# Kernel optimization log

Measured on AMD Instinct MI355X. Metric: run time of the kernel, lower is better.

## Reference

```python
import jax, jax.numpy as jnp
import numpy as np

B, S, H, E = 32, 4096, 512, 512
NEG = -1000000000.0


def setup_inputs() -> dict:
    key = jax.random.key(0)
    ks = jax.random.split(key, 8)
    query = jax.random.normal(ks[0], (B, H), dtype=jnp.float32)
    keys = jax.random.normal(ks[1], (B, S, E), dtype=jnp.float32)
    mask = jax.random.randint(ks[2], (B, S), 0, 2, dtype=jnp.int32)
    # learned params (torch Linear: y = x @ W.T + b); store W already transposed
    Wq = jax.random.normal(ks[3], (H, H), dtype=jnp.float32) / np.sqrt(H)
    bq = jnp.zeros((H,), dtype=jnp.float32)
    Wk = jax.random.normal(ks[4], (E, H), dtype=jnp.float32) / np.sqrt(E)
    bk = jnp.zeros((H,), dtype=jnp.float32)
    v = jax.random.normal(ks[5], (H,), dtype=jnp.float32) / np.sqrt(H)
    bv = jnp.zeros((), dtype=jnp.float32)
    return {"query": query, "keys": keys, "mask": mask,
            "Wq": Wq, "bq": bq, "Wk": Wk, "bk": bk, "v": v, "bv": bv}


def reference(query, keys, mask, Wq, bq, Wk, bk, v, bv):
    # q_proj: (B, 1, H); k_proj: (B, S, H)
    q_proj = (query @ Wq + bq)[:, None, :]
    k_proj = jnp.einsum('bse,eh->bsh', keys, Wk) + bk
    # additive score: v^T tanh(q + k) + bv -> (B, S)
    scores = jnp.einsum('bsh,h->bs', jnp.tanh(q_proj + k_proj), v) + bv
    scores = jnp.where(mask == 0, NEG, scores)
    attn = jax.nn.softmax(scores, axis=-1)          # (B, S)
    context = jnp.einsum('bs,bse->be', attn, keys)  # (B, E)
    return context, attn
```

## Files before the change

### kernel.cpp

```cpp
#include <hip/hip_runtime.h>
#include <hip/hip_bf16.h>

#define BB 32
#define SS 4096
#define HH 512
#define EE 512
#define NEGV -1000000000.0f

using float4v = __attribute__((ext_vector_type(4))) float;
using short8v = __attribute__((ext_vector_type(8))) short;
using short4v = __attribute__((ext_vector_type(4))) short;

__device__ inline unsigned short f2bf(float x) {
    union { float f; unsigned int u; } c; c.f = x;
    unsigned int r = c.u + 0x7FFFu + ((c.u >> 16) & 1u);
    return (unsigned short)(r >> 16);
}

__global__ void qproj_kernel(const float* __restrict__ query, const float* __restrict__ Wq,
                             float* __restrict__ qp) {
    __shared__ float qs[128];
    int b = blockIdx.y, e0 = blockIdx.x * 128, t = threadIdx.x;
    if (t < 128) qs[t] = query[b * HH + e0 + t];
    __syncthreads();
    int h0 = t, h1 = t + 256;
    float a0 = 0.f, a1 = 0.f;
    for (int e = 0; e < 128; ++e) {
        float q = qs[e];
        a0 += q * Wq[(size_t)(e0 + e) * HH + h0];
        a1 += q * Wq[(size_t)(e0 + e) * HH + h1];
    }
    atomicAdd(&qp[b * HH + h0], a0);
    atomicAdd(&qp[b * HH + h1], a1);
}

__global__ void wkt_kernel(const float* __restrict__ Wk, unsigned short* __restrict__ WkT) {
    int g = blockIdx.x * 256 + threadIdx.x;
    int lane = g & 63, nt = (g >> 6) & 31, ks = g >> 11;
    int lq = lane >> 4, lr = lane & 15;
    int h = nt * 16 + lr;
    int e0 = ks * 32 + lq * 8;
    short8v o;
    #pragma unroll
    for (int j = 0; j < 8; ++j) o[j] = (short)f2bf(Wk[(size_t)(e0 + j) * HH + h]);
    *(short8v*)(WkT + (size_t)g * 8) = o;
}

__launch_bounds__(512, 4)
__global__ void scores_kernel(const float* __restrict__ keys, const unsigned short* __restrict__ WkT,
                              const float* __restrict__ qp, const float* __restrict__ bq,
                              const float* __restrict__ bk, const float* __restrict__ v,
                              const float* __restrict__ bv, const int* __restrict__ mask,
                              float* __restrict__ scores) {
    constexpr int LDK = 264;
    __shared__ unsigned short klds[64 * LDK];
    __shared__ float qp_lds[HH];
    __shared__ float v_lds[HH];
    __shared__ float red[8][64];
    int b = blockIdx.y, s0 = blockIdx.x * 64;
    int tid = threadIdx.x;

    for (int i = tid; i < HH; i += 512) {
        qp_lds[i] = qp[b * HH + i] + bq[i] + bk[i];
        v_lds[i] = v[i];
    }

    int w = tid >> 6, lane = tid & 63;
    int lq = lane >> 4, lr = lane & 15;
    int nt0 = w * 4;

    float4v acc[4][4];
    #pragma unroll
    for (int m = 0; m < 4; ++m)
        #pragma unroll
        for (int j = 0; j < 4; ++j) acc[m][j] = (float4v){0.f, 0.f, 0.f, 0.f};

    const short8v* Wf = (const short8v*)WkT;

    for (int kc = 0; kc < 2; ++kc) {
        __syncthreads();
        const float4v* ksrc = (const float4v*)(keys + ((size_t)b * SS + s0) * EE + kc * 256);
        for (int i = tid; i < 64 * 64; i += 512) {
            int row = i >> 6, c4 = i & 63;
            float4v kv = ksrc[(size_t)row * 128 + c4];
            short4v p;
            p.x = (short)f2bf(kv.x); p.y = (short)f2bf(kv.y);
            p.z = (short)f2bf(kv.z); p.w = (short)f2bf(kv.w);
            *(short4v*)(&klds[row * LDK + c4 * 4]) = p;
        }
        __syncthreads();

        #pragma unroll
        for (int ks = 0; ks < 8; ++ks) {
            int ksg = kc * 8 + ks;
            short8v bfrag[4];
            #pragma unroll
            for (int j = 0; j < 4; ++j)
                bfrag[j] = Wf[((size_t)ksg * 32 + nt0 + j) * 64 + lane];
            #pragma unroll
            for (int m = 0; m < 4; ++m) {
                short8v afrag = *(const short8v*)(&klds[(m * 16 + lr) * LDK + ks * 32 + lq * 8]);
                #pragma unroll
                for (int j = 0; j < 4; ++j)
                    acc[m][j] = __builtin_amdgcn_mfma_f32_16x16x32_bf16(afrag, bfrag[j], acc[m][j], 0, 0, 0);
            }
        }
    }

    float part[4][4];
    #pragma unroll
    for (int m = 0; m < 4; ++m)
        #pragma unroll
        for (int r = 0; r < 4; ++r) part[m][r] = 0.f;
    #pragma unroll
    for (int j = 0; j < 4; ++j) {
        int h = (nt0 + j) * 16 + lr;
        float vj = v_lds[h], qj = qp_lds[h];
        #pragma unroll
        for (int m = 0; m < 4; ++m) {
            #pragma unroll
            for (int r = 0; r < 4; ++r) {
                float x = qj + acc[m][j][r];
                x = fminf(fmaxf(x, -12.f), 12.f);
                float e2 = __expf(2.f * x);
                part[m][r] += vj * ((e2 - 1.f) / (e2 + 1.f));
            }
        }
    }

    #pragma unroll
    for (int m = 0; m < 4; ++m)
        #pragma unroll
        for (int r = 0; r < 4; ++r) {
            float p = part[m][r];
            p += __shfl_xor(p, 1, 16);
            p += __shfl_xor(p, 2, 16);
            p += __shfl_xor(p, 4, 16);
            p += __shfl_xor(p, 8, 16);
            part[m][r] = p;
        }
    if (lr == 0) {
        #pragma unroll
        for (int m = 0; m < 4; ++m)
            #pragma unroll
            for (int r = 0; r < 4; ++r)
                red[w][m * 16 + lq * 4 + r] = part[m][r];
    }
    __syncthreads();
    if (tid < 64) {
        float sc = red[0][tid] + red[1][tid] + red[2][tid] + red[3][tid]
                 + red[4][tid] + red[5][tid] + red[6][tid] + red[7][tid] + bv[0];
        int s = s0 + tid;
        if (mask[b * SS + s] == 0) sc = NEGV;
        scores[b * SS + s] = sc;
    }
}

__global__ void softmax_kernel(const float* __restrict__ scores, float* __restrict__ attn) {
    __shared__ float red[1024];
    int b = blockIdx.x, t = threadIdx.x;
    float s_[4], e_[4];
    float lmax = -3e38f;
    #pragma unroll
    for (int i = 0; i < 4; ++i) { s_[i] = scores[b * SS + t + i * 1024]; lmax = fmaxf(lmax, s_[i]); }
    red[t] = lmax; __syncthreads();
    for (int off = 512; off > 0; off >>= 1) {
        if (t < off) red[t] = fmaxf(red[t], red[t + off]);
        __syncthreads();
    }
    float mx = red[0]; __syncthreads();
    float lsum = 0.f;
    #pragma unroll
    for (int i = 0; i < 4; ++i) { e_[i] = __expf(s_[i] - mx); lsum += e_[i]; }
    red[t] = lsum; __syncthreads();
    for (int off = 512; off > 0; off >>= 1) {
        if (t < off) red[t] += red[t + off];
        __syncthreads();
    }
    float inv = 1.f / red[0];
    #pragma unroll
    for (int i = 0; i < 4; ++i) attn[b * SS + t + i * 1024] = e_[i] * inv;
}

__launch_bounds__(256)
__global__ void context_kernel(const float* __restrict__ keys, const float* __restrict__ attn,
                               float* __restrict__ ctx) {
    __shared__ float a_s[128];
    int chunk = blockIdx.x, b = blockIdx.y, t = threadIdx.x;
    if (t < 128) a_s[t] = attn[b * SS + chunk * 128 + t];
    __syncthreads();
    const float* kbase = keys + ((size_t)b * SS + (size_t)chunk * 128) * EE;
    int e0 = (t & 127) * 4, sr = t >> 7;
    float4v a0 = (float4v){0.f,0.f,0.f,0.f}, a1 = a0, a2 = a0, a3 = a0;
    for (int ss = sr; ss < 128; ss += 8) {
        float4v k0 = *(const float4v*)(kbase + (size_t)(ss    ) * EE + e0);
        float4v k1 = *(const float4v*)(kbase + (size_t)(ss + 2) * EE + e0);
        float4v k2 = *(const float4v*)(kbase + (size_t)(ss + 4) * EE + e0);
        float4v k3 = *(const float4v*)(kbase + (size_t)(ss + 6) * EE + e0);
        float c0 = a_s[ss], c1 = a_s[ss + 2], c2 = a_s[ss + 4], c3 = a_s[ss + 6];
        a0.x += c0*k0.x; a0.y += c0*k0.y; a0.z += c0*k0.z; a0.w += c0*k0.w;
        a1.x += c1*k1.x; a1.y += c1*k1.y; a1.z += c1*k1.z; a1.w += c1*k1.w;
        a2.x += c2*k2.x; a2.y += c2*k2.y; a2.z += c2*k2.z; a2.w += c2*k2.w;
        a3.x += c3*k3.x; a3.y += c3*k3.y; a3.z += c3*k3.z; a3.w += c3*k3.w;
    }
    float4v s4;
    s4.x = (a0.x + a1.x) + (a2.x + a3.x);
    s4.y = (a0.y + a1.y) + (a2.y + a3.y);
    s4.z = (a0.z + a1.z) + (a2.z + a3.z);
    s4.w = (a0.w + a1.w) + (a2.w + a3.w);
    atomicAdd(&ctx[b * EE + e0 + 0], s4.x);
    atomicAdd(&ctx[b * EE + e0 + 1], s4.y);
    atomicAdd(&ctx[b * EE + e0 + 2], s4.z);
    atomicAdd(&ctx[b * EE + e0 + 3], s4.w);
}

extern "C" void kernel_launch(void* const* d_in, const int* in_sizes, int n_in,
                              void* d_out, int out_size, void* d_ws, size_t ws_size,
                              hipStream_t stream) {
    const float* query = (const float*)d_in[0];
    const float* keys  = (const float*)d_in[1];
    const int*   mask  = (const int*)d_in[2];
    const float* Wq    = (const float*)d_in[3];
    const float* bq    = (const float*)d_in[4];
    const float* Wk    = (const float*)d_in[5];
    const float* bk    = (const float*)d_in[6];
    const float* v     = (const float*)d_in[7];
    const float* bv    = (const float*)d_in[8];

    float* out  = (float*)d_out;
    float* ctx  = out;
    float* attn = out + BB * EE;

    char* ws = (char*)d_ws;
    float* qp = (float*)ws;
    unsigned short* WkT = (unsigned short*)(ws + 65536);
    float* scores = (float*)(ws + 65536 + 524288);

    hipMemsetAsync(ctx, 0, BB * EE * sizeof(float), stream);
    hipMemsetAsync(qp, 0, BB * HH * sizeof(float), stream);
    qproj_kernel<<<dim3(4, BB), 256, 0, stream>>>(query, Wq, qp);
    wkt_kernel<<<128, 256, 0, stream>>>(Wk, WkT);
    scores_kernel<<<dim3(SS / 64, BB), 512, 0, stream>>>(keys, WkT, qp, bq, bk, v, bv, mask, scores);
    softmax_kernel<<<BB, 1024, 0, stream>>>(scores, attn);
    context_kernel<<<dim3(SS / 128, BB), 256, 0, stream>>>(keys, attn, ctx);
}
```

Baseline: 509.2 us.

## Double-buffer keys tiles in scores kernel and deepen context/qproj unrolling

The scores kernel now splits the K dimension into four 128-wide chunks held in two LDS buffers. The next chunk's global loads are issued into registers before the current chunk's MFMAs and written to LDS afterwards, so global latency overlaps compute. Separately, the context kernel keeps 8 independent accumulators and loads for more memory-level parallelism, and qproj is split across twice as many blocks with an unrolled loop. This adds register pressure, which could reduce occupancy under the launch bounds.

```diff
diff --git a/kernel.cpp b/kernel.cpp
--- a/kernel.cpp
+++ b/kernel.cpp
@@ -19,13 +19,14 @@
 
 __global__ void qproj_kernel(const float* __restrict__ query, const float* __restrict__ Wq,
                              float* __restrict__ qp) {
-    __shared__ float qs[128];
-    int b = blockIdx.y, e0 = blockIdx.x * 128, t = threadIdx.x;
-    if (t < 128) qs[t] = query[b * HH + e0 + t];
+    __shared__ float qs[64];
+    int b = blockIdx.y, e0 = blockIdx.x * 64, t = threadIdx.x;
+    if (t < 64) qs[t] = query[b * HH + e0 + t];
     __syncthreads();
     int h0 = t, h1 = t + 256;
     float a0 = 0.f, a1 = 0.f;
-    for (int e = 0; e < 128; ++e) {
+    #pragma unroll 8
+    for (int e = 0; e < 64; ++e) {
         float q = qs[e];
         a0 += q * Wq[(size_t)(e0 + e) * HH + h0];
         a1 += q * Wq[(size_t)(e0 + e) * HH + h1];
@@ -52,8 +53,9 @@
                               const float* __restrict__ bk, const float* __restrict__ v,
                               const float* __restrict__ bv, const int* __restrict__ mask,
                               float* __restrict__ scores) {
-    constexpr int LDK = 264;
-    __shared__ unsigned short klds[64 * LDK];
+    constexpr int LDK = 136;
+    constexpr int BUF = 64 * LDK;
+    __shared__ unsigned short klds[2 * BUF];
     __shared__ float qp_lds[HH];
     __shared__ float v_lds[HH];
     __shared__ float red[8][64];
@@ -65,6 +67,22 @@
         v_lds[i] = v[i];
     }
 
+    const float4v* ksrc = (const float4v*)(keys + ((size_t)b * SS + s0) * EE);
+    int r0 = tid >> 5, c4 = tid & 31;
+
+    float4v kreg[4];
+    #pragma unroll
+    for (int p = 0; p < 4; ++p)
+        kreg[p] = ksrc[(size_t)(p * 16 + r0) * 128 + c4];
+    #pragma unroll
+    for (int p = 0; p < 4; ++p) {
+        short4v pk;
+        pk.x = (short)f2bf(kreg[p].x); pk.y = (short)f2bf(kreg[p].y);
+        pk.z = (short)f2bf(kreg[p].z); pk.w = (short)f2bf(kreg[p].w);
+        *(short4v*)(&klds[(p * 16 + r0) * LDK + c4 * 4]) = pk;
+    }
+    __syncthreads();
+
     int w = tid >> 6, lane = tid & 63;
     int lq = lane >> 4, lr = lane & 15;
     int nt0 = w * 4;
@@ -77,34 +95,39 @@
 
     const short8v* Wf = (const short8v*)WkT;
 
-    for (int kc = 0; kc < 2; ++kc) {
-        __syncthreads();
-        const float4v* ksrc = (const float4v*)(keys + ((size_t)b * SS + s0) * EE + kc * 256);
-        for (int i = tid; i < 64 * 64; i += 512) {
-            int row = i >> 6, c4 = i & 63;
-            float4v kv = ksrc[(size_t)row * 128 + c4];
-            short4v p;
-            p.x = (short)f2bf(kv.x); p.y = (short)f2bf(kv.y);
-            p.z = (short)f2bf(kv.z); p.w = (short)f2bf(kv.w);
-            *(short4v*)(&klds[row * LDK + c4 * 4]) = p;
-        }
-        __syncthreads();
-
-        #pragma unroll
-        for (int ks = 0; ks < 8; ++ks) {
-            int ksg = kc * 8 + ks;
+    for (int c = 0; c < 4; ++c) {
+        unsigned cur = (c & 1) * BUF;
+        if (c < 3) {
+            #pragma unroll
+            for (int p = 0; p < 4; ++p)
+                kreg[p] = ksrc[(size_t)(p * 16 + r0) * 128 + (c + 1) * 32 + c4];
+        }
+        #pragma unroll
+        for (int ks = 0; ks < 4; ++ks) {
+            int ksg = c * 4 + ks;
             short8v bfrag[4];
             #pragma unroll
             for (int j = 0; j < 4; ++j)
                 bfrag[j] = Wf[((size_t)ksg * 32 + nt0 + j) * 64 + lane];
             #pragma unroll
             for (int m = 0; m < 4; ++m) {
-                short8v afrag = *(const short8v*)(&klds[(m * 16 + lr) * LDK + ks * 32 + lq * 8]);
+                short8v afrag = *(const short8v*)(&klds[cur + (m * 16 + lr) * LDK + ks * 32 + lq * 8]);
                 #pragma unroll
                 for (int j = 0; j < 4; ++j)
                     acc[m][j] = __builtin_amdgcn_mfma_f32_16x16x32_bf16(afrag, bfrag[j], acc[m][j], 0, 0, 0);
             }
         }
+        if (c < 3) {
+            unsigned nxt = ((c + 1) & 1) * BUF;
+            #pragma unroll
+            for (int p = 0; p < 4; ++p) {
+                short4v pk;
+                pk.x = (short)f2bf(kreg[p].x); pk.y = (short)f2bf(kreg[p].y);
+                pk.z = (short)f2bf(kreg[p].z); pk.w = (short)f2bf(kreg[p].w);
+                *(short4v*)(&klds[nxt + (p * 16 + r0) * LDK + c4 * 4]) = pk;
+            }
+        }
+        __syncthreads();
     }
 
     float part[4][4];
@@ -191,23 +214,26 @@
     __syncthreads();
     const float* kbase = keys + ((size_t)b * SS + (size_t)chunk * 128) * EE;
     int e0 = (t & 127) * 4, sr = t >> 7;
-    float4v a0 = (float4v){0.f,0.f,0.f,0.f}, a1 = a0, a2 = a0, a3 = a0;
-    for (int ss = sr; ss < 128; ss += 8) {
-        float4v k0 = *(const float4v*)(kbase + (size_t)(ss    ) * EE + e0);
-        float4v k1 = *(const float4v*)(kbase + (size_t)(ss + 2) * EE + e0);
-        float4v k2 = *(const float4v*)(kbase + (size_t)(ss + 4) * EE + e0);
-        float4v k3 = *(const float4v*)(kbase + (size_t)(ss + 6) * EE + e0);
-        float c0 = a_s[ss], c1 = a_s[ss + 2], c2 = a_s[ss + 4], c3 = a_s[ss + 6];
-        a0.x += c0*k0.x; a0.y += c0*k0.y; a0.z += c0*k0.z; a0.w += c0*k0.w;
-        a1.x += c1*k1.x; a1.y += c1*k1.y; a1.z += c1*k1.z; a1.w += c1*k1.w;
-        a2.x += c2*k2.x; a2.y += c2*k2.y; a2.z += c2*k2.z; a2.w += c2*k2.w;
-        a3.x += c3*k3.x; a3.y += c3*k3.y; a3.z += c3*k3.z; a3.w += c3*k3.w;
+    float4v a[8];
+    #pragma unroll
+    for (int u = 0; u < 8; ++u) a[u] = (float4v){0.f, 0.f, 0.f, 0.f};
+    for (int ss = sr; ss < 128; ss += 16) {
+        float4v k[8];
+        #pragma unroll
+        for (int u = 0; u < 8; ++u)
+            k[u] = *(const float4v*)(kbase + (size_t)(ss + 2 * u) * EE + e0);
+        #pragma unroll
+        for (int u = 0; u < 8; ++u) {
+            float cw = a_s[ss + 2 * u];
+            a[u].x += cw * k[u].x; a[u].y += cw * k[u].y;
+            a[u].z += cw * k[u].z; a[u].w += cw * k[u].w;
+        }
     }
     float4v s4;
-    s4.x = (a0.x + a1.x) + (a2.x + a3.x);
-    s4.y = (a0.y + a1.y) + (a2.y + a3.y);
-    s4.z = (a0.z + a1.z) + (a2.z + a3.z);
-    s4.w = (a0.w + a1.w) + (a2.w + a3.w);
+    s4.x = ((a[0].x + a[1].x) + (a[2].x + a[3].x)) + ((a[4].x + a[5].x) + (a[6].x + a[7].x));
+    s4.y = ((a[0].y + a[1].y) + (a[2].y + a[3].y)) + ((a[4].y + a[5].y) + (a[6].y + a[7].y));
+    s4.z = ((a[0].z + a[1].z) + (a[2].z + a[3].z)) + ((a[4].z + a[5].z) + (a[6].z + a[7].z));
+    s4.w = ((a[0].w + a[1].w) + (a[2].w + a[3].w)) + ((a[4].w + a[5].w) + (a[6].w + a[7].w));
     atomicAdd(&ctx[b * EE + e0 + 0], s4.x);
     atomicAdd(&ctx[b * EE + e0 + 1], s4.y);
     atomicAdd(&ctx[b * EE + e0 + 2], s4.z);
@@ -238,7 +264,7 @@
 
     hipMemsetAsync(ctx, 0, BB * EE * sizeof(float), stream);
     hipMemsetAsync(qp, 0, BB * HH * sizeof(float), stream);
-    qproj_kernel<<<dim3(4, BB), 256, 0, stream>>>(query, Wq, qp);
+    qproj_kernel<<<dim3(8, BB), 256, 0, stream>>>(query, Wq, qp);
     wkt_kernel<<<128, 256, 0, stream>>>(Wk, WkT);
     scores_kernel<<<dim3(SS / 64, BB), 512, 0, stream>>>(keys, WkT, qp, bq, bk, v, bv, mask, scores);
     softmax_kernel<<<BB, 1024, 0, stream>>>(scores, attn);
```

New measurement: 487.7 us. 4.2% less time.

## Fuse scores, softmax and context into one pass with flash-style partial softmax

Applied to the files above, without the earlier changes.

The scores kernel now stages the full 64x512 key tile in LDS as bf16. It computes local softmax stats (max and sum) per 64-row chunk and accumulates an unnormalized partial context from the same LDS tile, so keys are read from HBM only once. A small finalize kernel rescales the chunk partials, writes ctx and attn, and replaces the separate softmax and context kernels and their atomics. This adds a bf16 rounding of keys in the context product, larger LDS use that lowers occupancy, and a tweak to the qproj split.

```diff
diff --git a/kernel.cpp b/kernel.cpp
--- a/kernel.cpp
+++ b/kernel.cpp
@@ -5,6 +5,7 @@
 #define SS 4096
 #define HH 512
 #define EE 512
+#define NCH 64
 #define NEGV -1000000000.0f
 
 using float4v = __attribute__((ext_vector_type(4))) float;
@@ -16,16 +17,21 @@
     unsigned int r = c.u + 0x7FFFu + ((c.u >> 16) & 1u);
     return (unsigned short)(r >> 16);
 }
+__device__ inline float bf2f(unsigned short s) {
+    union { float f; unsigned int u; } c; c.u = ((unsigned int)s) << 16;
+    return c.f;
+}
 
 __global__ void qproj_kernel(const float* __restrict__ query, const float* __restrict__ Wq,
                              float* __restrict__ qp) {
-    __shared__ float qs[128];
-    int b = blockIdx.y, e0 = blockIdx.x * 128, t = threadIdx.x;
-    if (t < 128) qs[t] = query[b * HH + e0 + t];
+    __shared__ float qs[64];
+    int b = blockIdx.y, e0 = blockIdx.x * 64, t = threadIdx.x;
+    if (t < 64) qs[t] = query[b * HH + e0 + t];
     __syncthreads();
     int h0 = t, h1 = t + 256;
     float a0 = 0.f, a1 = 0.f;
-    for (int e = 0; e < 128; ++e) {
+    #pragma unroll 8
+    for (int e = 0; e < 64; ++e) {
         float q = qs[e];
         a0 += q * Wq[(size_t)(e0 + e) * HH + h0];
         a1 += q * Wq[(size_t)(e0 + e) * HH + h1];
@@ -47,17 +53,19 @@
 }
 
 __launch_bounds__(512, 4)
-__global__ void scores_kernel(const float* __restrict__ keys, const unsigned short* __restrict__ WkT,
-                              const float* __restrict__ qp, const float* __restrict__ bq,
-                              const float* __restrict__ bk, const float* __restrict__ v,
-                              const float* __restrict__ bv, const int* __restrict__ mask,
-                              float* __restrict__ scores) {
-    constexpr int LDK = 264;
+__global__ void fused_kernel(const float* __restrict__ keys, const unsigned short* __restrict__ WkT,
+                             const float* __restrict__ qp, const float* __restrict__ bq,
+                             const float* __restrict__ bk, const float* __restrict__ v,
+                             const float* __restrict__ bv, const int* __restrict__ mask,
+                             float* __restrict__ scores, float* __restrict__ part,
+                             float* __restrict__ marr, float* __restrict__ larr) {
+    constexpr int LDK = EE + 8;
     __shared__ unsigned short klds[64 * LDK];
     __shared__ float qp_lds[HH];
     __shared__ float v_lds[HH];
     __shared__ float red[8][64];
-    int b = blockIdx.y, s0 = blockIdx.x * 64;
+    __shared__ float p_lds[64];
+    int b = blockIdx.y, c = blockIdx.x, s0 = c * 64;
     int tid = threadIdx.x;
 
     for (int i = tid; i < HH; i += 512) {
@@ -65,6 +73,24 @@
         v_lds[i] = v[i];
     }
 
+    const float4v* ksrc = (const float4v*)(keys + ((size_t)b * SS + s0) * EE);
+    #pragma unroll
+    for (int i0 = 0; i0 < 16; i0 += 4) {
+        float4v kv[4];
+        #pragma unroll
+        for (int p = 0; p < 4; ++p) kv[p] = ksrc[tid + (i0 + p) * 512];
+        #pragma unroll
+        for (int p = 0; p < 4; ++p) {
+            int idx = tid + (i0 + p) * 512;
+            int row = idx >> 7, c4 = idx & 127;
+            short4v pk;
+            pk.x = (short)f2bf(kv[p].x); pk.y = (short)f2bf(kv[p].y);
+            pk.z = (short)f2bf(kv[p].z); pk.w = (short)f2bf(kv[p].w);
+            *(short4v*)(&klds[row * LDK + c4 * 4]) = pk;
+        }
+    }
+    __syncthreads();
+
     int w = tid >> 6, lane = tid & 63;
     int lq = lane >> 4, lr = lane & 15;
     int nt0 = w * 4;
@@ -77,41 +103,26 @@
 
     const short8v* Wf = (const short8v*)WkT;
 
-    for (int kc = 0; kc < 2; ++kc) {
-        __syncthreads();
-        const float4v* ksrc = (const float4v*)(keys + ((size_t)b * SS + s0) * EE + kc * 256);
-        for (int i = tid; i < 64 * 64; i += 512) {
-            int row = i >> 6, c4 = i & 63;
-            float4v kv = ksrc[(size_t)row * 128 + c4];
-            short4v p;
-            p.x = (short)f2bf(kv.x); p.y = (short)f2bf(kv.y);
-            p.z = (short)f2bf(kv.z); p.w = (short)f2bf(kv.w);
-            *(short4v*)(&klds[row * LDK + c4 * 4]) = p;
-        }
-        __syncthreads();
-
-        #pragma unroll
-        for (int ks = 0; ks < 8; ++ks) {
-            int ksg = kc * 8 + ks;
-            short8v bfrag[4];
+    #pragma unroll 2
+    for (int ksg = 0; ksg < 16; ++ksg) {
+        short8v bfrag[4];
+        #pragma unroll
+        for (int j = 0; j < 4; ++j)
+            bfrag[j] = Wf[((size_t)ksg * 32 + nt0 + j) * 64 + lane];
+        #pragma unroll
+        for (int m = 0; m < 4; ++m) {
+            short8v afrag = *(const short8v*)(&klds[(m * 16 + lr) * LDK + ksg * 32 + lq * 8]);
             #pragma unroll
             for (int j = 0; j < 4; ++j)
-                bfrag[j] = Wf[((size_t)ksg * 32 + nt0 + j) * 64 + lane];
-            #pragma unroll
-            for (int m = 0; m < 4; ++m) {
-                short8v afrag = *(const short8v*)(&klds[(m * 16 + lr) * LDK + ks * 32 + lq * 8]);
-                #pragma unroll
-                for (int j = 0; j < 4; ++j)
-                    acc[m][j] = __builtin_amdgcn_mfma_f32_16x16x32_bf16(afrag, bfrag[j], acc[m][j], 0, 0, 0);
-            }
-        }
-    }
-
-    float part[4][4];
+                acc[m][j] = __builtin_amdgcn_mfma_f32_16x16x32_bf16(afrag, bfrag[j], acc[m][j], 0, 0, 0);
+        }
+    }
+
+    float part_r[4][4];
     #pragma unroll
     for (int m = 0; m < 4; ++m)
         #pragma unroll
-        for (int r = 0; r < 4; ++r) part[m][r] = 0.f;
+        for (int r = 0; r < 4; ++r) part_r[m][r] = 0.f;
     #pragma unroll
     for (int j = 0; j < 4; ++j) {
         int h = (nt0 + j) * 16 + lr;
@@ -123,95 +134,83 @@
                 float x = qj + acc[m][j][r];
                 x = fminf(fmaxf(x, -12.f), 12.f);
                 float e2 = __expf(2.f * x);
-                part[m][r] += vj * ((e2 - 1.f) / (e2 + 1.f));
+                part_r[m][r] += vj * ((e2 - 1.f) / (e2 + 1.f));
             }
         }
     }
-
     #pragma unroll
     for (int m = 0; m < 4; ++m)
         #pragma unroll
         for (int r = 0; r < 4; ++r) {
-            float p = part[m][r];
+            float p = part_r[m][r];
             p += __shfl_xor(p, 1, 16);
             p += __shfl_xor(p, 2, 16);
             p += __shfl_xor(p, 4, 16);
             p += __shfl_xor(p, 8, 16);
-            part[m][r] = p;
+            part_r[m][r] = p;
         }
     if (lr == 0) {
         #pragma unroll
         for (int m = 0; m < 4; ++m)
             #pragma unroll
             for (int r = 0; r < 4; ++r)
-                red[w][m * 16 + lq * 4 + r] = part[m][r];
-    }
-    __syncthreads();
+                red[w][m * 16 + lq * 4 + r] = part_r[m][r];
+    }
+    __syncthreads();
+
     if (tid < 64) {
         float sc = red[0][tid] + red[1][tid] + red[2][tid] + red[3][tid]
                  + red[4][tid] + red[5][tid] + red[6][tid] + red[7][tid] + bv[0];
         int s = s0 + tid;
         if (mask[b * SS + s] == 0) sc = NEGV;
         scores[b * SS + s] = sc;
-    }
-}
-
-__global__ void softmax_kernel(const float* __restrict__ scores, float* __restrict__ attn) {
-    __shared__ float red[1024];
+        float mv = sc;
+        #pragma unroll
+        for (int off = 1; off < 64; off <<= 1) mv = fmaxf(mv, __shfl_xor(mv, off));
+        float pe = __expf(sc - mv);
+        float ls = pe;
+        #pragma unroll
+        for (int off = 1; off < 64; off <<= 1) ls += __shfl_xor(ls, off);
+        p_lds[tid] = pe;
+        if (tid == 0) { marr[b * NCH + c] = mv; larr[b * NCH + c] = ls; }
+    }
+    __syncthreads();
+
+    float o = 0.f;
+    #pragma unroll 8
+    for (int s = 0; s < 64; ++s)
+        o += p_lds[s] * bf2f(klds[s * LDK + tid]);
+    part[((size_t)b * NCH + c) * EE + tid] = o;
+}
+
+__global__ void finalize_kernel(const float* __restrict__ scores, const float* __restrict__ part,
+                                const float* __restrict__ marr, const float* __restrict__ larr,
+                                float* __restrict__ ctx, float* __restrict__ attn) {
+    __shared__ float wgt[NCH];
+    __shared__ float Ms, Ls;
     int b = blockIdx.x, t = threadIdx.x;
-    float s_[4], e_[4];
-    float lmax = -3e38f;
-    #pragma unroll
-    for (int i = 0; i < 4; ++i) { s_[i] = scores[b * SS + t + i * 1024]; lmax = fmaxf(lmax, s_[i]); }
-    red[t] = lmax; __syncthreads();
-    for (int off = 512; off > 0; off >>= 1) {
-        if (t < off) red[t] = fmaxf(red[t], red[t + off]);
-        __syncthreads();
-    }
-    float mx = red[0]; __syncthreads();
-    float lsum = 0.f;
-    #pragma unroll
-    for (int i = 0; i < 4; ++i) { e_[i] = __expf(s_[i] - mx); lsum += e_[i]; }
-    red[t] = lsum; __syncthreads();
-    for (int off = 512; off > 0; off >>= 1) {
-        if (t < off) red[t] += red[t + off];
-        __syncthreads();
-    }
-    float inv = 1.f / red[0];
-    #pragma unroll
-    for (int i = 0; i < 4; ++i) attn[b * SS + t + i * 1024] = e_[i] * inv;
-}
-
-__launch_bounds__(256)
-__global__ void context_kernel(const float* __restrict__ keys, const float* __restrict__ attn,
-                               float* __restrict__ ctx) {
-    __shared__ float a_s[128];
-    int chunk = blockIdx.x, b = blockIdx.y, t = threadIdx.x;
-    if (t < 128) a_s[t] = attn[b * SS + chunk * 128 + t];
-    __syncthreads();
-    const float* kbase = keys + ((size_t)b * SS + (size_t)chunk * 128) * EE;
-    int e0 = (t & 127) * 4, sr = t >> 7;
-    float4v a0 = (float4v){0.f,0.f,0.f,0.f}, a1 = a0, a2 = a0, a3 = a0;
-    for (int ss = sr; ss < 128; ss += 8) {
-        float4v k0 = *(const float4v*)(kbase + (size_t)(ss    ) * EE + e0);
-        float4v k1 = *(const float4v*)(kbase + (size_t)(ss + 2) * EE + e0);
-        float4v k2 = *(const float4v*)(kbase + (size_t)(ss + 4) * EE + e0);
-        float4v k3 = *(const float4v*)(kbase + (size_t)(ss + 6) * EE + e0);
-        float c0 = a_s[ss], c1 = a_s[ss + 2], c2 = a_s[ss + 4], c3 = a_s[ss + 6];
-        a0.x += c0*k0.x; a0.y += c0*k0.y; a0.z += c0*k0.z; a0.w += c0*k0.w;
-        a1.x += c1*k1.x; a1.y += c1*k1.y; a1.z += c1*k1.z; a1.w += c1*k1.w;
-        a2.x += c2*k2.x; a2.y += c2*k2.y; a2.z += c2*k2.z; a2.w += c2*k2.w;
-        a3.x += c3*k3.x; a3.y += c3*k3.y; a3.z += c3*k3.z; a3.w += c3*k3.w;
-    }
-    float4v s4;
-    s4.x = (a0.x + a1.x) + (a2.x + a3.x);
-    s4.y = (a0.y + a1.y) + (a2.y + a3.y);
-    s4.z = (a0.z + a1.z) + (a2.z + a3.z);
-    s4.w = (a0.w + a1.w) + (a2.w + a3.w);
-    atomicAdd(&ctx[b * EE + e0 + 0], s4.x);
-    atomicAdd(&ctx[b * EE + e0 + 1], s4.y);
-    atomicAdd(&ctx[b * EE + e0 + 2], s4.z);
-    atomicAdd(&ctx[b * EE + e0 + 3], s4.w);
+    if (t < NCH) {
+        float m = marr[b * NCH + t], l = larr[b * NCH + t];
+        float M = m;
+        #pragma unroll
+        for (int off = 1; off < 64; off <<= 1) M = fmaxf(M, __shfl_xor(M, off));
+        float wq = __expf(m - M);
+        float L = wq * l;
+        #pragma unroll
+        for (int off = 1; off < 64; off <<= 1) L += __shfl_xor(L, off);
+        wgt[t] = wq;
+        if (t == 0) { Ms = M; Ls = L; }
+    }
+    __syncthreads();
+    float M = Ms, invL = 1.f / Ls;
+    float o = 0.f;
+    #pragma unroll 8
+    for (int cc = 0; cc < NCH; ++cc)
+        o += wgt[cc] * part[((size_t)b * NCH + cc) * EE + t];
+    ctx[b * EE + t] = o * invL;
+    #pragma unroll
+    for (int s = t; s < SS; s += 512)
+        attn[b * SS + s] = __expf(scores[b * SS + s] - M) * invL;
 }
 
 extern "C" void kernel_launch(void* const* d_in, const int* in_sizes, int n_in,
@@ -232,15 +231,17 @@
     float* attn = out + BB * EE;
 
     char* ws = (char*)d_ws;
-    float* qp = (float*)ws;
+    float* qp           = (float*)ws;
     unsigned short* WkT = (unsigned short*)(ws + 65536);
-    float* scores = (float*)(ws + 65536 + 524288);
-
-    hipMemsetAsync(ctx, 0, BB * EE * sizeof(float), stream);
+    float* scores       = (float*)(ws + 589824);
+    float* part         = (float*)(ws + 1114112);
+    float* marr         = (float*)(ws + 5308416);
+    float* larr         = (float*)(ws + 5316608);
+
     hipMemsetAsync(qp, 0, BB * HH * sizeof(float), stream);
-    qproj_kernel<<<dim3(4, BB), 256, 0, stream>>>(query, Wq, qp);
+    qproj_kernel<<<dim3(8, BB), 256, 0, stream>>>(query, Wq, qp);
     wkt_kernel<<<128, 256, 0, stream>>>(Wk, WkT);
-    scores_kernel<<<dim3(SS / 64, BB), 512, 0, stream>>>(keys, WkT, qp, bq, bk, v, bv, mask, scores);
-    softmax_kernel<<<BB, 1024, 0, stream>>>(scores, attn);
-    context_kernel<<<dim3(SS / 128, BB), 256, 0, stream>>>(keys, attn, ctx);
-}
+    fused_kernel<<<dim3(NCH, BB), 512, 0, stream>>>(keys, WkT, qp, bq, bk, v, bv, mask,
+                                                    scores, part, marr, larr);
+    finalize_kernel<<<BB, 512, 0, stream>>>(scores, part, marr, larr, ctx, attn);
+}
```

After: 445.1 us. 1.14x faster.
